# Kernel tuning notes

Measured on AMD Instinct MI355X. Metric: run time of the kernel, lower is better.

Reference implementation:

```python
import jax, jax.numpy as jnp
import numpy as np

NUM_EMBEDDINGS = 8192
EMBEDDING_DIM = 256
COMMITMENT_WEIGHT = 0.25
EMA_DECAY = 0.99
EPSILON = 1e-05


def setup_inputs() -> dict:
    key = jax.random.key(0)
    k1, k2 = jax.random.split(key)
    z = jax.random.normal(k1, (8, 4096, EMBEDDING_DIM), dtype=jnp.float32)
    # xavier-uniform-ish codebook init
    limit = np.sqrt(6.0 / (NUM_EMBEDDINGS + EMBEDDING_DIM))
    embeddings = jax.random.uniform(
        k2, (NUM_EMBEDDINGS, EMBEDDING_DIM), dtype=jnp.float32,
        minval=-limit, maxval=limit)
    ema_cluster_size = jnp.zeros((NUM_EMBEDDINGS,), dtype=jnp.float32)
    ema_embed_sum = embeddings.copy()
    return {
        'z': z,
        'embeddings': embeddings,
        'ema_cluster_size': ema_cluster_size,
        'ema_embed_sum': ema_embed_sum,
    }


def reference(z, embeddings, ema_cluster_size, ema_embed_sum):
    input_shape = z.shape
    D = input_shape[-1]
    z_flat = z.reshape(-1, D)                                  # [N, D]

    # Squared euclidean distances via expansion: ||z||^2 + ||e||^2 - 2 z.e
    z_sq = jnp.sum(z_flat * z_flat, axis=1, keepdims=True)     # [N, 1]
    e_sq = jnp.sum(embeddings * embeddings, axis=1)            # [K]
    ze = jnp.matmul(z_flat, embeddings.T)                      # [N, K]
    distances = z_sq + e_sq - 2.0 * ze                          # [N, K]
    indices = jnp.argmin(distances, axis=1)                    # [N] int

    z_q_flat = embeddings[indices]                             # [N, D] gather
    z_q = z_q_flat.reshape(input_shape)

    # commitment loss = mse(stop_grad(z_q), z)
    diff = jax.lax.stop_gradient(z_q) - z
    commitment_loss = jnp.mean(diff * diff) * COMMITMENT_WEIGHT

    # straight-through estimator
    z_q_st = z + jax.lax.stop_gradient(z_q - z)

    # EMA codebook update (functional version of the in-place buffer update)
    ones = jnp.ones_like(indices, dtype=embeddings.dtype)
    cluster_size = jax.ops.segment_sum(ones, indices, num_segments=NUM_EMBEDDINGS)
    embed_sum = jax.ops.segment_sum(z_flat, indices, num_segments=NUM_EMBEDDINGS)
    new_ema_cluster_size = EMA_DECAY * ema_cluster_size + (1.0 - EMA_DECAY) * cluster_size
    new_ema_embed_sum = EMA_DECAY * ema_embed_sum + (1.0 - EMA_DECAY) * embed_sum
    new_embeddings = new_ema_embed_sum / (new_ema_cluster_size[:, None] + EPSILON)

    indices_out = indices.reshape(input_shape[:-1])
    return (z_q_st, indices_out, commitment_loss,
            new_embeddings, new_ema_cluster_size, new_ema_embed_sum)
```

## Files before the change

kernel.cpp:

```cpp
#include <hip/hip_runtime.h>
#include <hip/hip_bf16.h>
#include <math.h>

#define N_TOK   32768
#define DIM     256
#define KC      8192

#define OUT_ZQ    0
#define OUT_IDX   8388608
#define OUT_LOSS  8421376
#define OUT_NEMB  8421377
#define OUT_CS    10518529
#define OUT_SUM   10526721

#define MARGIN  8e-3f
#define FLAGCAP 16384

typedef __attribute__((ext_vector_type(8))) __bf16 bf16x8;
typedef __attribute__((ext_vector_type(4))) float f32x4;

__device__ __forceinline__ void gload16(const void* g, void* l) {
  __builtin_amdgcn_global_load_lds((const __attribute__((address_space(1))) void*)g,
                                   (__attribute__((address_space(3))) void*)l, 16, 0, 0);
}

__device__ __forceinline__ float np_sumsq256(const float* __restrict__ p, int lane) {
  const int l = lane & 15;
  const int h = l >> 3;
  const int j = l & 7;
  const float* a = p + h * 128 + j;
  float x = a[0];
  float r = __fmul_rn(x, x);
  #pragma unroll
  for (int i = 1; i < 16; ++i) {
    x = a[8 * i];
    r = __fadd_rn(r, __fmul_rn(x, x));
  }
  r = __fadd_rn(r, __shfl_down(r, 1));
  r = __fadd_rn(r, __shfl_down(r, 2));
  r = __fadd_rn(r, __shfl_down(r, 4));
  float hi = __shfl(r, (lane & 48) | 8);
  return __fadd_rn(r, hi);
}

__global__ void vq_prep(const float* __restrict__ emb, float* __restrict__ esq,
                        short* __restrict__ esp2, int* __restrict__ hist,
                        int* __restrict__ cnt) {
  const int t = threadIdx.x;
  const int code = blockIdx.x * 8 + (t >> 5);
  const int p = t & 31, j = p >> 2, g = p & 3;
  const float* src = emb + (size_t)code * DIM + j * 32 + g * 8;
  const float4 v0 = *(const float4*)src;
  const float4 v1 = *(const float4*)(src + 4);
  const float xf[8] = {v0.x, v0.y, v0.z, v0.w, v1.x, v1.y, v1.z, v1.w};
  bf16x8 hb;
  #pragma unroll
  for (int e = 0; e < 8; ++e) hb[e] = (__bf16)xf[e];
  const int c = code & 15, sub = (code >> 4) & 3, ct = code >> 6;
  const int slot = (g + (c >> 1)) & 3;
  char* dst = (char*)esp2 + (size_t)ct * 32768 + ((sub * 8 + j) << 10) + c * 64 + slot * 16;
  *(bf16x8*)dst = hb;
  if (t < 128) {
    const int code2 = blockIdx.x * 8 + (t >> 4);
    const float s = np_sumsq256(emb + (size_t)code2 * DIM, t & 63);
    if ((t & 15) == 0) esq[code2] = s;
  }
  if (blockIdx.x < 32) hist[blockIdx.x * 256 + t] = 0;
  if (blockIdx.x == 0 && t == 0) cnt[0] = 0;
}

__global__ void vq_transpose(const float* __restrict__ emb, float* __restrict__ embT) {
  __shared__ float t[64][65];
  const int tid = threadIdx.x;
  const int bc  = blockIdx.x & 127;
  const int bk  = blockIdx.x >> 7;
  const int cc0 = bc << 6, kc0 = bk << 6;
  const int col = tid & 63, qr = tid >> 6;
  #pragma unroll
  for (int i = 0; i < 16; ++i) {
    const int row = i * 4 + qr;
    t[row][col] = emb[(size_t)(cc0 + row) * DIM + kc0 + col];
  }
  __syncthreads();
  #pragma unroll
  for (int i = 0; i < 16; ++i) {
    const int krow = i * 4 + qr;
    embT[(size_t)(kc0 + krow) * KC + cc0 + col] = t[col][krow];
  }
}

__launch_bounds__(256, 4)
__global__ void vq_mfma(const float* __restrict__ z,
                        const short* __restrict__ esp,
                        const float* __restrict__ esq,
                        float* __restrict__ pb1,
                        int* __restrict__ pi1,
                        float* __restrict__ pb2) {
  __shared__ __align__(16) char lds[32768];
  const int tid  = threadIdx.x;
  const int lane = tid & 63;
  const int w    = tid >> 6;
  const int l15  = lane & 15;
  const int g    = lane >> 4;
  const int rt   = blockIdx.x >> 2;
  const int kh   = blockIdx.x & 3;
  const int rowbase = rt * 128 + w * 32;
  const int u0 = kh * 64, u1 = u0 + 64;
  const int gx = (g + (l15 >> 1)) & 3;
  const char* espb = (const char*)esp;

#define STAGE(U, BUFB)                                                           \
  {                                                                              \
    _Pragma("unroll")                                                            \
    for (int q_ = 0; q_ < 4; ++q_) {                                             \
      const int so_ = (((w << 2) + q_) << 10);                                   \
      gload16(espb + (size_t)(U) * 16384 + so_ + (lane << 4),                    \
              (void*)(lds + (BUFB) + so_));                                      \
    }                                                                            \
  }

  STAGE(u0, 0);

  bf16x8 Ahi[2][8];
  #pragma unroll
  for (int s = 0; s < 2; ++s) {
    const float* zr = z + (size_t)(rowbase + s * 16 + l15) * DIM + g * 8;
    #pragma unroll
    for (int c = 0; c < 8; ++c) {
      const float4 v0 = *(const float4*)(zr + c * 32);
      const float4 v1 = *(const float4*)(zr + c * 32 + 4);
      const float xf[8] = {v0.x, v0.y, v0.z, v0.w, v1.x, v1.y, v1.z, v1.w};
      #pragma unroll
      for (int e = 0; e < 8; ++e) Ahi[s][c][e] = (__bf16)xf[e];
    }
  }

  __syncthreads();

  float b1[2][4], b2[2][4];
  int   i1[2][4];
  #pragma unroll
  for (int s = 0; s < 2; ++s)
    #pragma unroll
    for (int r = 0; r < 4; ++r) { b1[s][r] = 3.4e38f; b2[s][r] = 3.4e38f; i1[s][r] = 0x7fffffff; }

  int bp = 0;
  for (int u = u0; u < u1; ++u) {
    if (u + 1 < u1) STAGE(u + 1, (bp ^ 1) << 14);

    const float eq0 = esq[(u << 5) + l15];
    const float eq1 = esq[(u << 5) + 16 + l15];

    f32x4 acc00 = (f32x4){0.f, 0.f, 0.f, 0.f};
    f32x4 acc01 = (f32x4){0.f, 0.f, 0.f, 0.f};
    f32x4 acc10 = (f32x4){0.f, 0.f, 0.f, 0.f};
    f32x4 acc11 = (f32x4){0.f, 0.f, 0.f, 0.f};

    {
      const char* base = lds + (bp << 14);
      #pragma unroll
      for (int j_ = 0; j_ < 8; ++j_) {
        const char* bq_ = base + (j_ << 10) + (l15 << 6) + (gx << 4);
        const bf16x8 bF0 = *(const bf16x8*)(bq_);
        const bf16x8 bF1 = *(const bf16x8*)(bq_ + 8192);
        acc00 = __builtin_amdgcn_mfma_f32_16x16x32_bf16(Ahi[0][j_], bF0, acc00, 0, 0, 0);
        acc01 = __builtin_amdgcn_mfma_f32_16x16x32_bf16(Ahi[0][j_], bF1, acc01, 0, 0, 0);
        acc10 = __builtin_amdgcn_mfma_f32_16x16x32_bf16(Ahi[1][j_], bF0, acc10, 0, 0, 0);
        acc11 = __builtin_amdgcn_mfma_f32_16x16x32_bf16(Ahi[1][j_], bF1, acc11, 0, 0, 0);
      }
    }

    const int code0 = (u << 5) + l15;
    const int code1 = code0 + 16;
    #pragma unroll
    for (int r = 0; r < 4; ++r) {
      const float sc = fmaf(-2.f, acc00[r], eq0);
      const bool lt = sc < b1[0][r];
      b2[0][r] = fminf(b2[0][r], fmaxf(sc, b1[0][r]));
      i1[0][r] = lt ? code0 : i1[0][r];
      b1[0][r] = fminf(b1[0][r], sc);
    }
    #pragma unroll
    for (int r = 0; r < 4; ++r) {
      const float sc = fmaf(-2.f, acc01[r], eq1);
      const bool lt = sc < b1[0][r];
      b2[0][r] = fminf(b2[0][r], fmaxf(sc, b1[0][r]));
      i1[0][r] = lt ? code1 : i1[0][r];
      b1[0][r] = fminf(b1[0][r], sc);
    }
    #pragma unroll
    for (int r = 0; r < 4; ++r) {
      const float sc = fmaf(-2.f, acc10[r], eq0);
      const bool lt = sc < b1[1][r];
      b2[1][r] = fminf(b2[1][r], fmaxf(sc, b1[1][r]));
      i1[1][r] = lt ? code0 : i1[1][r];
      b1[1][r] = fminf(b1[1][r], sc);
    }
    #pragma unroll
    for (int r = 0; r < 4; ++r) {
      const float sc = fmaf(-2.f, acc11[r], eq1);
      const bool lt = sc < b1[1][r];
      b2[1][r] = fminf(b2[1][r], fmaxf(sc, b1[1][r]));
      i1[1][r] = lt ? code1 : i1[1][r];
      b1[1][r] = fminf(b1[1][r], sc);
    }
    __syncthreads();
    bp ^= 1;
  }

  #pragma unroll
  for (int s = 0; s < 2; ++s) {
    #pragma unroll
    for (int r = 0; r < 4; ++r) {
      float v1 = b1[s][r], v2 = b2[s][r];
      int   j1 = i1[s][r];
      #pragma unroll
      for (int off = 1; off < 16; off <<= 1) {
        const float o1 = __shfl_xor(v1, off);
        const int   oj = __shfl_xor(j1, off);
        const float o2 = __shfl_xor(v2, off);
        v2 = fminf(fminf(v2, o2), fmaxf(v1, o1));
        const bool tk = (o1 < v1) || (o1 == v1 && oj < j1);
        j1 = tk ? oj : j1;
        v1 = fminf(v1, o1);
      }
      if (l15 == 0) {
        const int rr = kh * N_TOK + rowbase + s * 16 + (g << 2) + r;
        pb1[rr] = v1; pi1[rr] = j1; pb2[rr] = v2;
      }
    }
  }
}

__global__ void vq_merge(const float* __restrict__ pb1, const int* __restrict__ pi1,
                         const float* __restrict__ pb2, int* __restrict__ idxf,
                         int* __restrict__ flag, int* __restrict__ cnt) {
  const int gi = blockIdx.x * blockDim.x + threadIdx.x;
  float v1 = pb1[gi], v2 = pb2[gi];
  int   i1 = pi1[gi];
  #pragma unroll
  for (int h = 1; h < 4; ++h) {
    const float o1 = pb1[h * N_TOK + gi];
    const int   oj = pi1[h * N_TOK + gi];
    const float o2 = pb2[h * N_TOK + gi];
    if (o1 < v1 || (o1 == v1 && oj < i1)) {
      v2 = fminf(v1, o2);
      v1 = o1; i1 = oj;
    } else {
      v2 = fminf(v2, o1);
    }
  }
  idxf[gi] = i1;
  if (v2 - v1 < MARGIN) {
    const int p = atomicAdd(cnt, 1);
    if (p < FLAGCAP) flag[p] = gi;
  }
}

__global__ void vq_rescan2(const float* __restrict__ z,
                           const float* __restrict__ embT,
                           const float* __restrict__ esq,
                           const int* __restrict__ flag,
                           const int* __restrict__ cnt,
                           float* __restrict__ rpv,
                           int* __restrict__ rpi) {
  __shared__ __align__(16) float zT[DIM][16];
  __shared__ float zsq_sh[16];
  __shared__ float rv[4][16];
  __shared__ int   ri[4][16];
  __shared__ int   rown[16];
  int n = *cnt; if (n > FLAGCAP) n = FLAGCAP;
  const int tid = threadIdx.x;
  const int lane = tid & 63, wv = tid >> 6;
  const int nb = (n + 15) >> 4;
  const int ntask = nb * 8;
  for (int task = blockIdx.x; task < ntask; task += gridDim.x) {
    const int bb = task >> 3, cz = task & 7;
    __syncthreads();
    if (tid < 16) rown[tid] = flag[min(bb * 16 + tid, n - 1)];
    __syncthreads();
    #pragma unroll
    for (int rr = 0; rr < 16; ++rr) zT[tid][rr] = z[(size_t)rown[rr] * DIM + tid];
    {
      const int rr = tid >> 4;
      const float s = np_sumsq256(z + (size_t)rown[rr] * DIM, lane);
      if ((tid & 15) == 0) zsq_sh[rr] = s;
    }
    __syncthreads();

    float a[16][4];
    #pragma unroll
    for (int rr = 0; rr < 16; ++rr)
      #pragma unroll
      for (int q = 0; q < 4; ++q) a[rr][q] = 0.f;

    const int c0 = cz * 1024 + tid;
    #pragma unroll 2
    for (int k = 0; k < DIM; ++k) {
      const float* rk = embT + (size_t)k * KC + c0;
      const float e0 = rk[0], e1 = rk[256], e2 = rk[512], e3 = rk[768];
      const f32x4 z0 = *(const f32x4*)&zT[k][0];
      const f32x4 z1 = *(const f32x4*)&zT[k][4];
      const f32x4 z2 = *(const f32x4*)&zT[k][8];
      const f32x4 z3 = *(const f32x4*)&zT[k][12];
      #pragma unroll
      for (int r4 = 0; r4 < 4; ++r4) {
        a[r4][0] = fmaf(z0[r4], e0, a[r4][0]);
        a[r4][1] = fmaf(z0[r4], e1, a[r4][1]);
        a[r4][2] = fmaf(z0[r4], e2, a[r4][2]);
        a[r4][3] = fmaf(z0[r4], e3, a[r4][3]);
        a[4 + r4][0] = fmaf(z1[r4], e0, a[4 + r4][0]);
        a[4 + r4][1] = fmaf(z1[r4], e1, a[4 + r4][1]);
        a[4 + r4][2] = fmaf(z1[r4], e2, a[4 + r4][2]);
        a[4 + r4][3] = fmaf(z1[r4], e3, a[4 + r4][3]);
        a[8 + r4][0] = fmaf(z2[r4], e0, a[8 + r4][0]);
        a[8 + r4][1] = fmaf(z2[r4], e1, a[8 + r4][1]);
        a[8 + r4][2] = fmaf(z2[r4], e2, a[8 + r4][2]);
        a[8 + r4][3] = fmaf(z2[r4], e3, a[8 + r4][3]);
        a[12 + r4][0] = fmaf(z3[r4], e0, a[12 + r4][0]);
        a[12 + r4][1] = fmaf(z3[r4], e1, a[12 + r4][1]);
        a[12 + r4][2] = fmaf(z3[r4], e2, a[12 + r4][2]);
        a[12 + r4][3] = fmaf(z3[r4], e3, a[12 + r4][3]);
      }
    }

    #pragma unroll
    for (int rr = 0; rr < 16; ++rr) {
      float bv = 3.4e38f; int bi = 0x7fffffff;
      #pragma unroll
      for (int q = 0; q < 4; ++q) {
        const int code = cz * 1024 + q * 256 + tid;
        const float D = __fsub_rn(__fadd_rn(zsq_sh[rr], esq[code]), __fmul_rn(2.f, a[rr][q]));
        if (D < bv) { bv = D; bi = code; }
      }
      #pragma unroll
      for (int off = 32; off; off >>= 1) {
        const float ov = __shfl_down(bv, off);
        const int   oi = __shfl_down(bi, off);
        if (ov < bv || (ov == bv && oi < bi)) { bv = ov; bi = oi; }
      }
      if (lane == 0) { rv[wv][rr] = bv; ri[wv][rr] = bi; }
    }
    __syncthreads();
    if (tid < 16) {
      const int fi = bb * 16 + tid;
      if (fi < n) {
        float fv = rv[0][tid]; int fx = ri[0][tid];
        #pragma unroll
        for (int q = 1; q < 4; ++q)
          if (rv[q][tid] < fv || (rv[q][tid] == fv && ri[q][tid] < fx)) { fv = rv[q][tid]; fx = ri[q][tid]; }
        rpv[fi * 8 + cz] = fv; rpi[fi * 8 + cz] = fx;
      }
    }
  }
}

__global__ void vq_rmerge(const int* __restrict__ flag, const int* __restrict__ cnt,
                          const float* __restrict__ rpv, const int* __restrict__ rpi,
                          int* __restrict__ idxf) {
  int n = *cnt; if (n > FLAGCAP) n = FLAGCAP;
  const int fi = blockIdx.x * blockDim.x + threadIdx.x;
  if (fi >= n) return;
  float bv = rpv[fi * 8]; int bi = rpi[fi * 8];
  #pragma unroll
  for (int c = 1; c < 8; ++c) {
    const float v = rpv[fi * 8 + c]; const int ix = rpi[fi * 8 + c];
    if (v < bv || (v == bv && ix < bi)) { bv = v; bi = ix; }
  }
  idxf[flag[fi]] = bi;
}

__global__ void vq_gather(const float* __restrict__ z, const float* __restrict__ emb,
                          const int* __restrict__ idxf, float* __restrict__ out,
                          float* __restrict__ lossp, int* __restrict__ hist) {
  __shared__ float part[4];
  const int tid = threadIdx.x, lane = tid & 63, w = tid >> 6;
  const int row = blockIdx.x * 4 + w;
  const int code = idxf[row];
  const float4 zv = *(const float4*)(z + (size_t)row * DIM + lane * 4);
  const float4 ev = *(const float4*)(emb + (size_t)code * DIM + lane * 4);
  float4 d, o;
  d.x = ev.x - zv.x; d.y = ev.y - zv.y; d.z = ev.z - zv.z; d.w = ev.w - zv.w;
  o.x = zv.x + d.x;  o.y = zv.y + d.y;  o.z = zv.z + d.z;  o.w = zv.w + d.w;
  *(float4*)(out + OUT_ZQ + (size_t)row * DIM + lane * 4) = o;
  float sq = fmaf(d.x, d.x, fmaf(d.y, d.y, fmaf(d.z, d.z, d.w * d.w)));
  #pragma unroll
  for (int off = 32; off; off >>= 1) sq += __shfl_down(sq, off);
  if (lane == 0) {
    part[w] = sq;
    atomicAdd(hist + code, 1);
    out[OUT_IDX + row] = (float)code;
  }
  __syncthreads();
  if (tid == 0) lossp[blockIdx.x] = (part[0] + part[1]) + (part[2] + part[3]);
}

__global__ void vq_prefix(const float* __restrict__ ema_cs, int* __restrict__ hist,
                          int* __restrict__ base, int* __restrict__ cursor,
                          const float* __restrict__ lossp, float* __restrict__ out) {
  __shared__ int ps[256];
  __shared__ float lp[4];
  const int t = threadIdx.x;

  float ls = 0.f;
  #pragma unroll
  for (int j = 0; j < 8; ++j) {
    const float4 v = *(const float4*)(lossp + t * 32 + j * 4);
    ls += (v.x + v.y) + (v.z + v.w);
  }
  #pragma unroll
  for (int off = 32; off; off >>= 1) ls += __shfl_down(ls, off);
  if ((t & 63) == 0) lp[t >> 6] = ls;

  int loc[32]; int s = 0;
  #pragma unroll
  for (int j = 0; j < 32; ++j) { loc[j] = hist[t * 32 + j]; s += loc[j]; }
  ps[t] = s;
  __syncthreads();
  if (t == 0)
    out[OUT_LOSS] = 0.25f * (((lp[0] + lp[1]) + (lp[2] + lp[3])) * (1.f / 8388608.f));
  for (int off = 1; off < 256; off <<= 1) {
    const int v = (t >= off) ? ps[t - off] : 0;
    __syncthreads();
    ps[t] += v;
    __syncthreads();
  }
  int run = ps[t] - s;
  #pragma unroll
  for (int j = 0; j < 32; ++j) {
    const int i = t * 32 + j;
    base[i] = run; cursor[i] = run;
    out[OUT_CS + i] = 0.99f * ema_cs[i] + 0.01f * (float)loc[j];
    run += loc[j];
  }
}

__global__ void vq_slot(const int* __restrict__ idxf, int* __restrict__ cursor,
                        int* __restrict__ rowlist) {
  const int gi = blockIdx.x * blockDim.x + threadIdx.x;
  const int code = idxf[gi];
  const int p = atomicAdd(cursor + code, 1);
  rowlist[p] = gi;
}

__global__ void vq_embsum(const float* __restrict__ z, const float* __restrict__ ema_sum,
                          const int* __restrict__ rowlist, const int* __restrict__ base,
                          const int* __restrict__ hist, float* __restrict__ out) {
  const int code = blockIdx.x;
  const int lane = threadIdx.x;
  const int b = base[code], n = hist[code];
  float a0 = 0.f, a1 = 0.f, a2 = 0.f, a3 = 0.f;
  for (int i = 0; i < n; ++i) {
    const float4 v = *(const float4*)(z + (size_t)rowlist[b + i] * DIM + lane * 4);
    a0 += v.x; a1 += v.y; a2 += v.z; a3 += v.w;
  }
  const float4 es = *(const float4*)(ema_sum + (size_t)code * DIM + lane * 4);
  const float s0 = 0.99f * es.x + 0.01f * a0;
  const float s1 = 0.99f * es.y + 0.01f * a1;
  const float s2 = 0.99f * es.z + 0.01f * a2;
  const float s3 = 0.99f * es.w + 0.01f * a3;
  float* sp = out + OUT_SUM + (size_t)code * DIM + lane * 4;
  sp[0] = s0; sp[1] = s1; sp[2] = s2; sp[3] = s3;
  const float cs = out[OUT_CS + code] + 1e-5f;
  float* np_ = out + OUT_NEMB + (size_t)code * DIM + lane * 4;
  np_[0] = s0 / cs; np_[1] = s1 / cs; np_[2] = s2 / cs; np_[3] = s3 / cs;
}

extern "C" void kernel_launch(void* const* d_in, const int* in_sizes, int n_in,
                              void* d_out, int out_size, void* d_ws, size_t ws_size,
                              hipStream_t stream) {
  const float* z      = (const float*)d_in[0];
  const float* emb    = (const float*)d_in[1];
  const float* emacs  = (const float*)d_in[2];
  const float* emasum = (const float*)d_in[3];
  float* out = (float*)d_out;
  float* ws  = (float*)d_ws;

  float* esq     = ws;
  int*   idxf    = (int*)(ws + 8192);
  int*   flag    = (int*)(ws + 40960);
  int*   cnt     = (int*)(ws + 57344);
  int*   hist    = (int*)(ws + 57600);
  int*   base    = (int*)(ws + 65792);
  int*   cursor  = (int*)(ws + 73984);
  int*   rowlist = (int*)(ws + 82176);
  float* pb1     = ws + 114944;
  int*   pi1     = (int*)(ws + 246016);
  float* pb2     = ws + 377088;
  short* esp2    = (short*)(ws + 508160);
  float* embT    = ws + 1556736;
  float* rpv     = ws + 3653888;
  int*   rpi     = (int*)(ws + 3784960);
  float* lossp   = pb1;

  vq_prep<<<KC / 8, 256, 0, stream>>>(emb, esq, esp2, hist, cnt);
  vq_transpose<<<512, 256, 0, stream>>>(emb, embT);

  vq_mfma<<<1024, 256, 0, stream>>>(z, esp2, esq, pb1, pi1, pb2);
  vq_merge<<<N_TOK / 256, 256, 0, stream>>>(pb1, pi1, pb2, idxf, flag, cnt);
  vq_rescan2<<<1024, 256, 0, stream>>>(z, embT, esq, flag, cnt, rpv, rpi);
  vq_rmerge<<<FLAGCAP / 256, 256, 0, stream>>>(flag, cnt, rpv, rpi, idxf);

  vq_gather<<<N_TOK / 4, 256, 0, stream>>>(z, emb, idxf, out, lossp, hist);
  vq_prefix<<<1, 256, 0, stream>>>(emacs, hist, base, cursor, lossp, out);
  vq_slot<<<N_TOK / 256, 256, 0, stream>>>(idxf, cursor, rowlist);
  vq_embsum<<<KC, 64, 0, stream>>>(z, emasum, rowlist, base, hist, out);
}
```

Measured before the change: 331.6 us.

## Fuse z_q write and commitment loss into per-code embsum pass

Removes the separate gather kernel, which read z and the codebook per row to write z_q and loss partials. The embsum kernel, which already reads each z row once per code, now also writes the code vector as z_q and accumulates the squared difference. A small histogram kernel and a separate loss-reduction kernel replace the old pieces. This saves a full read of z, at the cost of scattered z_q writes and one extra launch; load imbalance across codes may grow.

```diff
diff --git a/kernel.cpp b/kernel.cpp
--- a/kernel.cpp
+++ b/kernel.cpp
@@ -370,55 +370,24 @@
   idxf[flag[fi]] = bi;
 }
 
-__global__ void vq_gather(const float* __restrict__ z, const float* __restrict__ emb,
-                          const int* __restrict__ idxf, float* __restrict__ out,
-                          float* __restrict__ lossp, int* __restrict__ hist) {
-  __shared__ float part[4];
-  const int tid = threadIdx.x, lane = tid & 63, w = tid >> 6;
-  const int row = blockIdx.x * 4 + w;
-  const int code = idxf[row];
-  const float4 zv = *(const float4*)(z + (size_t)row * DIM + lane * 4);
-  const float4 ev = *(const float4*)(emb + (size_t)code * DIM + lane * 4);
-  float4 d, o;
-  d.x = ev.x - zv.x; d.y = ev.y - zv.y; d.z = ev.z - zv.z; d.w = ev.w - zv.w;
-  o.x = zv.x + d.x;  o.y = zv.y + d.y;  o.z = zv.z + d.z;  o.w = zv.w + d.w;
-  *(float4*)(out + OUT_ZQ + (size_t)row * DIM + lane * 4) = o;
-  float sq = fmaf(d.x, d.x, fmaf(d.y, d.y, fmaf(d.z, d.z, d.w * d.w)));
-  #pragma unroll
-  for (int off = 32; off; off >>= 1) sq += __shfl_down(sq, off);
-  if (lane == 0) {
-    part[w] = sq;
-    atomicAdd(hist + code, 1);
-    out[OUT_IDX + row] = (float)code;
-  }
-  __syncthreads();
-  if (tid == 0) lossp[blockIdx.x] = (part[0] + part[1]) + (part[2] + part[3]);
+__global__ void vq_hist(const int* __restrict__ idxf, int* __restrict__ hist,
+                        float* __restrict__ out) {
+  const int gi = blockIdx.x * blockDim.x + threadIdx.x;
+  const int code = idxf[gi];
+  atomicAdd(hist + code, 1);
+  out[OUT_IDX + gi] = (float)code;
 }
 
 __global__ void vq_prefix(const float* __restrict__ ema_cs, int* __restrict__ hist,
                           int* __restrict__ base, int* __restrict__ cursor,
-                          const float* __restrict__ lossp, float* __restrict__ out) {
+                          float* __restrict__ out) {
   __shared__ int ps[256];
-  __shared__ float lp[4];
   const int t = threadIdx.x;
-
-  float ls = 0.f;
-  #pragma unroll
-  for (int j = 0; j < 8; ++j) {
-    const float4 v = *(const float4*)(lossp + t * 32 + j * 4);
-    ls += (v.x + v.y) + (v.z + v.w);
-  }
-  #pragma unroll
-  for (int off = 32; off; off >>= 1) ls += __shfl_down(ls, off);
-  if ((t & 63) == 0) lp[t >> 6] = ls;
-
   int loc[32]; int s = 0;
   #pragma unroll
   for (int j = 0; j < 32; ++j) { loc[j] = hist[t * 32 + j]; s += loc[j]; }
   ps[t] = s;
   __syncthreads();
-  if (t == 0)
-    out[OUT_LOSS] = 0.25f * (((lp[0] + lp[1]) + (lp[2] + lp[3])) * (1.f / 8388608.f));
   for (int off = 1; off < 256; off <<= 1) {
     const int v = (t >= off) ? ps[t - off] : 0;
     __syncthreads();
@@ -443,17 +412,27 @@
   rowlist[p] = gi;
 }
 
-__global__ void vq_embsum(const float* __restrict__ z, const float* __restrict__ ema_sum,
+__global__ void vq_embsum(const float* __restrict__ z, const float* __restrict__ emb,
+                          const float* __restrict__ ema_sum,
                           const int* __restrict__ rowlist, const int* __restrict__ base,
-                          const int* __restrict__ hist, float* __restrict__ out) {
+                          const int* __restrict__ hist, float* __restrict__ out,
+                          float* __restrict__ lossp) {
   const int code = blockIdx.x;
   const int lane = threadIdx.x;
   const int b = base[code], n = hist[code];
-  float a0 = 0.f, a1 = 0.f, a2 = 0.f, a3 = 0.f;
+  const float4 ev = *(const float4*)(emb + (size_t)code * DIM + lane * 4);
+  float a0 = 0.f, a1 = 0.f, a2 = 0.f, a3 = 0.f, ls = 0.f;
   for (int i = 0; i < n; ++i) {
-    const float4 v = *(const float4*)(z + (size_t)rowlist[b + i] * DIM + lane * 4);
+    const int row = rowlist[b + i];
+    const float4 v = *(const float4*)(z + (size_t)row * DIM + lane * 4);
     a0 += v.x; a1 += v.y; a2 += v.z; a3 += v.w;
-  }
+    const float d0 = ev.x - v.x, d1 = ev.y - v.y, d2 = ev.z - v.z, d3 = ev.w - v.w;
+    ls = fmaf(d0, d0, fmaf(d1, d1, fmaf(d2, d2, fmaf(d3, d3, ls))));
+    *(float4*)(out + OUT_ZQ + (size_t)row * DIM + lane * 4) = ev;
+  }
+  #pragma unroll
+  for (int off = 32; off; off >>= 1) ls += __shfl_down(ls, off);
+  if (lane == 0) lossp[code] = ls;
   const float4 es = *(const float4*)(ema_sum + (size_t)code * DIM + lane * 4);
   const float s0 = 0.99f * es.x + 0.01f * a0;
   const float s1 = 0.99f * es.y + 0.01f * a1;
@@ -464,6 +443,23 @@
   const float cs = out[OUT_CS + code] + 1e-5f;
   float* np_ = out + OUT_NEMB + (size_t)code * DIM + lane * 4;
   np_[0] = s0 / cs; np_[1] = s1 / cs; np_[2] = s2 / cs; np_[3] = s3 / cs;
+}
+
+__global__ void vq_lossred(const float* __restrict__ lossp, float* __restrict__ out) {
+  __shared__ float lp[4];
+  const int t = threadIdx.x;
+  float ls = 0.f;
+  #pragma unroll
+  for (int j = 0; j < 8; ++j) {
+    const float4 v = *(const float4*)(lossp + t * 32 + j * 4);
+    ls += (v.x + v.y) + (v.z + v.w);
+  }
+  #pragma unroll
+  for (int off = 32; off; off >>= 1) ls += __shfl_down(ls, off);
+  if ((t & 63) == 0) lp[t >> 6] = ls;
+  __syncthreads();
+  if (t == 0)
+    out[OUT_LOSS] = 0.25f * (((lp[0] + lp[1]) + (lp[2] + lp[3])) * (1.f / 8388608.f));
 }
 
 extern "C" void kernel_launch(void* const* d_in, const int* in_sizes, int n_in,
@@ -501,8 +497,9 @@
   vq_rescan2<<<1024, 256, 0, stream>>>(z, embT, esq, flag, cnt, rpv, rpi);
   vq_rmerge<<<FLAGCAP / 256, 256, 0, stream>>>(flag, cnt, rpv, rpi, idxf);
 
-  vq_gather<<<N_TOK / 4, 256, 0, stream>>>(z, emb, idxf, out, lossp, hist);
-  vq_prefix<<<1, 256, 0, stream>>>(emacs, hist, base, cursor, lossp, out);
+  vq_hist<<<N_TOK / 256, 256, 0, stream>>>(idxf, hist, out);
+  vq_prefix<<<1, 256, 0, stream>>>(emacs, hist, base, cursor, out);
   vq_slot<<<N_TOK / 256, 256, 0, stream>>>(idxf, cursor, rowlist);
-  vq_embsum<<<KC, 64, 0, stream>>>(z, emasum, rowlist, base, hist, out);
-}
+  vq_embsum<<<KC, 64, 0, stream>>>(z, emb, emasum, rowlist, base, hist, out, lossp);
+  vq_lossred<<<1, 256, 0, stream>>>(lossp, out);
+}
```

After: 327.7 us. About the same (-1.2%).
